# Kernel optimization log

Measured on AMD Instinct MI355X. Metric: run time of the kernel, lower is better.

## Reference

```python
import jax, jax.numpy as jnp
import numpy as np

N_ORDER = 256
PRED_LEN = 192
SEQ_LEN = 768
ENC_IN = 21
BATCH = 16
MULTISCALE = [1, 2, 4]
MODES = 32  # min(32, min(pred_len, seq_len)//2)


def _transition(N):
    Q = np.arange(N, dtype=np.float64)
    R = (2 * Q + 1)[:, None]
    j, i = np.meshgrid(Q, Q)
    A = np.where(i < j, -1, (-1.0) ** (i - j + 1)) * R
    B = (-1.0) ** Q[:, None] * R
    return A, B


def _bilinear(A, B, dt):
    # scipy cont2discrete(method='bilinear'): Ad=(I-dt/2 A)^-1 (I+dt/2 A), Bd=(I-dt/2 A)^-1 dt B
    N = A.shape[0]
    I = np.eye(N)
    ima = I - (dt / 2.0) * A
    Ad = np.linalg.solve(ima, I + (dt / 2.0) * A)
    Bd = np.linalg.solve(ima, dt * B)
    return Ad, Bd.squeeze(-1)


def _legendre_eval(N, x):
    # Legendre P_n(x) via three-term recurrence; returns [len(x), N]
    T = x.shape[0]
    P = np.zeros((N, T))
    P[0] = 1.0
    if N > 1:
        P[1] = x
    for n in range(2, N):
        P[n] = ((2 * n - 1) * x * P[n - 1] - (n - 1) * P[n - 2]) / n
    return P.T


def setup_inputs() -> dict:
    key = jax.random.key(0)
    ks = jax.random.split(key, 12)
    inp = {"x_enc": jax.random.normal(ks[0], (BATCH, SEQ_LEN, ENC_IN), dtype=jnp.float32)}
    Ac, Bc = _transition(N_ORDER)
    scale = 1.0 / (N_ORDER * N_ORDER)
    for idx, m in enumerate(MULTISCALE):
        dt = 1.0 / PRED_LEN / m
        Ad, Bd = _bilinear(Ac, Bc, dt)
        vals = np.arange(0.0, 1.0, dt)
        E = _legendre_eval(N_ORDER, 1.0 - 2.0 * vals)
        inp[f"A{idx}"] = jnp.asarray(Ad, jnp.float32)
        inp[f"B{idx}"] = jnp.asarray(Bd, jnp.float32)
        inp[f"E{idx}"] = jnp.asarray(E, jnp.float32)
        inp[f"Wr{idx}"] = scale * jax.random.uniform(ks[1 + 2 * idx], (N_ORDER, N_ORDER, MODES), dtype=jnp.float32)
        inp[f"Wi{idx}"] = scale * jax.random.uniform(ks[2 + 2 * idx], (N_ORDER, N_ORDER, MODES), dtype=jnp.float32)
    inp["mlp_w"] = 0.1 * jax.random.normal(ks[10], (1, len(MULTISCALE)), dtype=jnp.float32)
    inp["mlp_b"] = jnp.zeros((1,), jnp.float32)
    return inp


def _hippo(x, A, Bv):
    # x: [B, E, L]; c_t = c_{t-1} @ A^T + f_t * B  (F.linear(c, A) == c @ A.T)
    def step(c, f):
        c = c @ A.T + f[..., None] * Bv
        return c, c
    c0 = jnp.zeros(x.shape[:-1] + (A.shape[0],), x.dtype)
    _, cs = jax.lax.scan(step, c0, jnp.moveaxis(x, -1, 0))
    return jnp.moveaxis(cs, 0, -1)  # [B, E, N, L]


def _spec_conv(x, Wr, Wi):
    # x: [B, E, N_in, L]; keep first MODES rfft modes, complex channel mix, irfft
    L = x.shape[-1]
    a = jnp.fft.rfft(x, axis=-1)[..., :MODES]
    W = (Wr + 1j * Wi).astype(jnp.complex64)
    out = jnp.einsum('bjix,iox->bjox', a, W)
    nf = L // 2 + 1
    out_full = jnp.pad(out, ((0, 0), (0, 0), (0, 0), (0, nf - MODES)))
    return jnp.fft.irfft(out_full, n=L, axis=-1)


def reference(x_enc, A0, B0, E0, Wr0, Wi0, A1, B1, E1, Wr1, Wi1, A2, B2, E2, Wr2, Wi2, mlp_w, mlp_b):
    params = [(A0, B0, E0, Wr0, Wi0), (A1, B1, E1, Wr1, Wi1), (A2, B2, E2, Wr2, Wi2)]
    x_decs = []
    for m, (A, Bv, E, Wr, Wi) in zip(MULTISCALE, params):
        x_in = x_enc[:, -m * PRED_LEN:]                      # [B, L, E]
        c = _hippo(jnp.transpose(x_in, (0, 2, 1)), A, Bv)    # [B, E, N, L]
        out1 = _spec_conv(c, Wr, Wi)                         # [B, E, N, L]
        x_dec_c = out1[:, :, :, PRED_LEN - 1]                # seq_len >= pred_len, jump_dist=0
        x_decs.append(x_dec_c @ E[-PRED_LEN:].T)             # [B, E, pred_len]
    x_dec = jnp.stack(x_decs, axis=-1)                       # [B, E, pred_len, 3]
    out = x_dec @ mlp_w[0] + mlp_b[0]                        # Linear(3,1) then squeeze
    return jnp.transpose(out, (0, 2, 1))                     # [B, pred_len, E]
```

## Files before the change

### kernel.cpp

```cpp
#include <hip/hip_runtime.h>
#include <math.h>

#define PI_F 3.14159265358979323846f

#define W_OFF    0
#define AP_OFF   344064
#define KT_OFF   737280
#define KTOT_OFF 995328
#define Y_OFF    1142784
#define S_OFF    1142784
#define F_OFF    1732608
#define QT_OFF   10579968
#define WS_FLOATS 27095040

__device__ __forceinline__ int off_w_f(int s)  { return 49152  * ((1 << s) - 1); }
__device__ __forceinline__ int qoff_f(int s)   { return 2359296 * ((1 << s) - 1); }
__device__ __forceinline__ int foff_f(int s)   { return 1179648 * ((1 << s) - 1); }

template<bool BT>
__device__ __forceinline__ void gemm_tile32(const float* __restrict__ A,
                                            const float* __restrict__ B,
                                            float* __restrict__ C,
                                            int M, int ldc, int m0, int n0)
{
    __shared__ float As[16][36];
    __shared__ float Bs[16][68];
    const int tid = threadIdx.x;
    const int tx = tid & 15;
    const int ty = tid >> 4;

    float acc[2][4] = {{0.f,0.f,0.f,0.f},{0.f,0.f,0.f,0.f}};

    for (int kk = 0; kk < 256; kk += 16) {
        if (tid < 128) {
            int r  = tid >> 2;
            int kq = (tid & 3) << 2;
            float4 av = make_float4(0.f, 0.f, 0.f, 0.f);
            if (m0 + r < M)
                av = *(const float4*)(A + (size_t)(m0 + r) * 256 + kk + kq);
            As[kq + 0][r] = av.x; As[kq + 1][r] = av.y;
            As[kq + 2][r] = av.z; As[kq + 3][r] = av.w;
        }
        if (BT) {
            int rb = tid >> 2;
            int kq = (tid & 3) << 2;
            float4 bv = *(const float4*)(B + (size_t)(n0 + rb) * 256 + kk + kq);
            Bs[kq + 0][rb] = bv.x; Bs[kq + 1][rb] = bv.y;
            Bs[kq + 2][rb] = bv.z; Bs[kq + 3][rb] = bv.w;
        } else {
            int kb = tid >> 4;
            int j4 = (tid & 15) << 2;
            float4 bv = *(const float4*)(B + (size_t)(kk + kb) * 256 + n0 + j4);
            *(float4*)(&Bs[kb][j4]) = bv;
        }
        __syncthreads();

        #pragma unroll
        for (int kq = 0; kq < 16; ++kq) {
            float a0 = As[kq][2 * ty];
            float a1 = As[kq][2 * ty + 1];
            float4 b4 = *(const float4*)(&Bs[kq][tx << 2]);
            acc[0][0] = fmaf(a0, b4.x, acc[0][0]);
            acc[0][1] = fmaf(a0, b4.y, acc[0][1]);
            acc[0][2] = fmaf(a0, b4.z, acc[0][2]);
            acc[0][3] = fmaf(a0, b4.w, acc[0][3]);
            acc[1][0] = fmaf(a1, b4.x, acc[1][0]);
            acc[1][1] = fmaf(a1, b4.y, acc[1][1]);
            acc[1][2] = fmaf(a1, b4.z, acc[1][2]);
            acc[1][3] = fmaf(a1, b4.w, acc[1][3]);
        }
        __syncthreads();
    }

    #pragma unroll
    for (int u = 0; u < 2; ++u) {
        int row = m0 + 2 * ty + u;
        if (row < M) {
            float4 cv = make_float4(acc[u][0], acc[u][1], acc[u][2], acc[u][3]);
            *(float4*)(C + (size_t)row * ldc + n0 + (tx << 2)) = cv;
        }
    }
}

__device__ __forceinline__ void gemm64x128_q(const float* __restrict__ A,
                                             const float* __restrict__ B,
                                             float* __restrict__ C, int ldc)
{
    __shared__ float As[16][68];
    __shared__ float Bs[16][132];

    const int tid = threadIdx.x;
    const int tx = tid & 15;
    const int ty = tid >> 4;
    const int ra  = tid >> 2;
    const int kqa = (tid & 3) << 2;
    const int rb  = tid >> 1;
    const int kq8 = (tid & 1) << 3;

    float acc[2][4][4];
    #pragma unroll
    for (int g = 0; g < 2; ++g)
        #pragma unroll
        for (int u = 0; u < 4; ++u)
            #pragma unroll
            for (int v = 0; v < 4; ++v) acc[g][u][v] = 0.f;

    for (int kk = 0; kk < 256; kk += 16) {
        float4 av = *(const float4*)(A + (size_t)ra * 256 + kk + kqa);
        As[kqa + 0][ra] = av.x; As[kqa + 1][ra] = av.y;
        As[kqa + 2][ra] = av.z; As[kqa + 3][ra] = av.w;

        const float* bp = B + (size_t)rb * 256 + kk + kq8;
        float4 b0 = *(const float4*)(bp);
        float4 b1 = *(const float4*)(bp + 4);
        Bs[kq8 + 0][rb] = b0.x; Bs[kq8 + 1][rb] = b0.y;
        Bs[kq8 + 2][rb] = b0.z; Bs[kq8 + 3][rb] = b0.w;
        Bs[kq8 + 4][rb] = b1.x; Bs[kq8 + 5][rb] = b1.y;
        Bs[kq8 + 6][rb] = b1.z; Bs[kq8 + 7][rb] = b1.w;
        __syncthreads();

        #pragma unroll
        for (int kq = 0; kq < 16; ++kq) {
            float4 a   = *(const float4*)(&As[kq][4 * ty]);
            float4 b0v = *(const float4*)(&Bs[kq][4 * tx]);
            float4 b1v = *(const float4*)(&Bs[kq][4 * tx + 64]);
            float af[4] = {a.x, a.y, a.z, a.w};
            float bf[8] = {b0v.x, b0v.y, b0v.z, b0v.w, b1v.x, b1v.y, b1v.z, b1v.w};
            #pragma unroll
            for (int g = 0; g < 2; ++g)
                #pragma unroll
                for (int u = 0; u < 4; ++u)
                    #pragma unroll
                    for (int v = 0; v < 4; ++v)
                        acc[g][u][v] = fmaf(af[u], bf[g * 4 + v], acc[g][u][v]);
        }
        __syncthreads();
    }

    #pragma unroll
    for (int u = 0; u < 4; ++u) {
        int row = 4 * ty + u;
        #pragma unroll
        for (int g = 0; g < 2; ++g) {
            float4 cv = make_float4(acc[g][u][0], acc[g][u][1],
                                    acc[g][u][2], acc[g][u][3]);
            *(float4*)(C + (size_t)row * ldc + 4 * tx + 64 * g) = cv;
        }
    }
}

__global__ void k_level2(int n, int sbase, const float* A0, const float* A1,
                         const float* A2, const float* B0, const float* B1,
                         const float* B2, float* ws)
{
    int s = blockIdx.z + sbase;
    int L = 192 << s;
    const float* Ain = (s == 0) ? A0 : (s == 1) ? A1 : A2;
    const float* Bv  = (s == 0) ? B0 : (s == 1) ? B1 : B2;
    float* wbase = ws + W_OFF + off_w_f(s);
    float* bufA  = ws + AP_OFF + s * 131072;
    float* bufB  = bufA + 65536;
    const float* src = (n == 0) ? Ain : (((n - 1) & 1) ? bufB : bufA);

    const int y = blockIdx.y;
    const int n0col = blockIdx.x * 64;

    if (n == 0 && y == 15 && blockIdx.x == 3)
        ws[W_OFF + off_w_f(s) + threadIdx.x] = Bv[threadIdx.x];

    if (y < 8) {
        int p2 = 1 << n;
        if (p2 >= L) return;
        int cnt = min(p2, L - p2);
        int m0 = y * 32;
        if (m0 >= cnt) return;
        const float* Aop = (n == 0) ? Bv : wbase;
        gemm_tile32<true>(Aop, src, wbase + (size_t)p2 * 256, cnt, 256, m0, n0col);
    } else {
        if ((2 << n) >= L) return;
        float* dst = (n & 1) ? bufB : bufA;
        gemm_tile32<false>(src, src, dst, 256, 256, (y - 8) * 32, n0col);
    }
}

__global__ void k_transpose(const float* Wr0, const float* Wi0,
                            const float* Wr1, const float* Wi1,
                            const float* Wr2, const float* Wi2, float* ws)
{
    __shared__ float t[256][33];
    int bid = blockIdx.x;
    int i  = bid & 255;
    int ri = (bid >> 8) & 1;
    int s  = bid >> 9;
    const float* W;
    if (s == 0)      W = ri ? Wi0 : Wr0;
    else if (s == 1) W = ri ? Wi1 : Wr1;
    else             W = ri ? Wi2 : Wr2;

    const int tid = threadIdx.x;
    const float* slab = W + (size_t)i * 8192;
    #pragma unroll
    for (int j = 0; j < 8; ++j) {
        int f = j * 1024 + tid * 4;
        float4 v = *(const float4*)(slab + f);
        int o = f >> 5;
        int k = f & 31;
        t[o][k + 0] = v.x; t[o][k + 1] = v.y;
        t[o][k + 2] = v.z; t[o][k + 3] = v.w;
    }
    __syncthreads();

    int sri = s * 2 + ri;
    #pragma unroll
    for (int k = 0; k < 32; ++k) {
        ws[QT_OFF + (size_t)(sri * 32 + k) * 65536 + (size_t)i * 256 + tid] = t[tid][k];
    }
}

__global__ void __launch_bounds__(256, 4)
k_gemm_Y5(const float* E0, const float* E1, const float* E2, float* __restrict__ ws)
{
    const int z  = blockIdx.z;
    const int s  = z >> 6;
    const int L  = 192 << s;
    const int n0 = blockIdx.x * 128;
    const int m0 = blockIdx.y * 64;
    const float* E = (s == 0) ? E0 : (s == 1) ? E1 : E2;

    const float* Ap = E + (size_t)(L - 192) * 256 + (size_t)m0 * 256;
    const float* Bp = ws + QT_OFF + (size_t)z * 65536 + (size_t)n0 * 256;
    float* Cp = ws + Y_OFF + (size_t)z * 49152 + (size_t)m0 * 256 + n0;
    gemm64x128_q(Ap, Bp, Cp, 256);
}

__global__ void __launch_bounds__(256, 4)
k_gemm_Q4(float* __restrict__ ws)
{
    const int y = blockIdx.y;
    int s, yt;
    if (y < 3)      { s = 0; yt = y; }
    else if (y < 9) { s = 1; yt = y - 3; }
    else            { s = 2; yt = y - 9; }
    const int m0 = yt * 64;
    const int n0 = blockIdx.x * 128;

    const float* Ap = ws + W_OFF + off_w_f(s) + (size_t)m0 * 256;
    const float* Bp = ws + Y_OFF + (size_t)s * 3145728 + (size_t)n0 * 256;
    float* Cp = ws + QT_OFF + qoff_f(s) + (size_t)m0 * 12288 + n0;
    gemm64x128_q(Ap, Bp, Cp, 12288);
}

__global__ void k_scanA(float* __restrict__ ws)
{
    const int c = blockIdx.x;
    const int k = blockIdx.y;
    const int s = blockIdx.z;
    const int L = 192 << s;
    const int C = L >> 4;
    const int p = threadIdx.x;

    __shared__ float twc[768], tws[768];
    for (int m = p; m < L; m += 192) {
        float ang = -2.f * PI_F * (float)m / (float)L;
        float ss, cc; sincosf(ang, &ss, &cc);
        twc[m] = cc; tws[m] = ss;
    }
    __syncthreads();

    const float* Qr = ws + QT_OFF + qoff_f(s) + (size_t)k * 192;
    const float* Qi = Qr + 6144;

    float ar = 0.f, ai = 0.f;
    const int d0 = c * C;
    int ph = (k * d0) % L;
    for (int j = 0; j < C; ++j) {
        int d = d0 + j;
        float qr = Qr[(size_t)d * 12288 + p];
        float qi = Qi[(size_t)d * 12288 + p];
        float cc = twc[ph], sn = tws[ph];
        ar = fmaf(cc, qr, fmaf(-sn, qi, ar));
        ai = fmaf(cc, qi, fmaf( sn, qr, ai));
        ph += k; if (ph >= L) ph -= L;
    }
    size_t sb = (size_t)((s * 32 + k) * 16 + c) * 384;
    ws[S_OFF + sb + p]       = ar;
    ws[S_OFF + sb + 192 + p] = ai;
}

__global__ void k_scanB(float* __restrict__ ws)
{
    const int c = blockIdx.x;
    const int k = blockIdx.y;
    const int s = blockIdx.z;
    const int L = 192 << s;
    const int C = L >> 4;
    const int p = threadIdx.x;

    __shared__ float twc[768], tws[768];
    for (int m = p; m < L; m += 192) {
        float ang = -2.f * PI_F * (float)m / (float)L;
        float ss, cc; sincosf(ang, &ss, &cc);
        twc[m] = cc; tws[m] = ss;
    }
    __syncthreads();

    float ar = 0.f, ai = 0.f;
    size_t sbase = (size_t)(s * 32 + k) * 16 * 384;
    for (int c2 = 0; c2 < c; ++c2) {
        ar += ws[S_OFF + sbase + (size_t)c2 * 384 + p];
        ai += ws[S_OFF + sbase + (size_t)c2 * 384 + 192 + p];
    }

    const float ck = ((k == 0) ? 1.f : 2.f) / (float)L;
    const float* Qr = ws + QT_OFF + qoff_f(s) + (size_t)k * 192;
    const float* Qi = Qr + 6144;
    float* F = ws + F_OFF + foff_f(s);

    const int d0 = c * C;
    int ph = (k * d0) % L;
    int m1 = d0 + 192 - L; if (m1 < 0) m1 += L;
    int ph2 = (k * m1) % L;
    for (int j = 0; j < C; ++j) {
        int d = d0 + j;
        float qr = Qr[(size_t)d * 12288 + p];
        float qi = Qi[(size_t)d * 12288 + p];
        float cc = twc[ph], sn = tws[ph];
        ar = fmaf(cc, qr, fmaf(-sn, qi, ar));
        ai = fmaf(cc, qi, fmaf( sn, qr, ai));
        float f = ck * fmaf(twc[ph2], ar, tws[ph2] * ai);
        int sidx = L - 1 - d;
        F[((size_t)sidx * 32 + k) * 192 + p] = f;
        ph  += k; if (ph  >= L) ph  -= L;
        ph2 += k; if (ph2 >= L) ph2 -= L;
    }
}

__global__ void k_kredc(float* __restrict__ ws, const float* __restrict__ mw)
{
    const int tau = blockIdx.x;
    const int p   = threadIdx.x;
    float sum = 0.f;
    #pragma unroll
    for (int s = 0; s < 3; ++s) {
        int L = 192 << s;
        int off = 768 - L;
        if (tau >= off) {
            int sidx = tau - off;
            const float* F = ws + F_OFF + foff_f(s) + (size_t)sidx * 32 * 192;
            float kt = 0.f;
            #pragma unroll
            for (int k = 0; k < 32; ++k)
                kt += F[k * 192 + p];
            sum = fmaf(mw[s], kt, sum);
        }
    }
    ws[KTOT_OFF + (size_t)tau * 192 + p] = sum;
}

__global__ void k_out(const float* __restrict__ x, const float* __restrict__ ws,
                      const float* __restrict__ mb, float* __restrict__ out)
{
    int bid = blockIdx.x;
    int b = bid / 21;
    int c = bid - b * 21;
    __shared__ float xl[768];
    for (int t = threadIdx.x; t < 768; t += 192)
        xl[t] = x[((size_t)b * 768 + t) * 21 + c];
    __syncthreads();

    int p = threadIdx.x;
    const float* K = ws + KTOT_OFF;
    float acc = 0.f;
    for (int tau = 0; tau < 768; ++tau)
        acc = fmaf(xl[tau], K[(size_t)tau * 192 + p], acc);
    out[((size_t)b * 192 + p) * 21 + c] = acc + mb[0];
}

extern "C" void kernel_launch(void* const* d_in, const int* in_sizes, int n_in,
                              void* d_out, int out_size, void* d_ws, size_t ws_size,
                              hipStream_t stream)
{
    const float* x   = (const float*)d_in[0];
    const float* A0  = (const float*)d_in[1];
    const float* B0  = (const float*)d_in[2];
    const float* E0  = (const float*)d_in[3];
    const float* Wr0 = (const float*)d_in[4];
    const float* Wi0 = (const float*)d_in[5];
    const float* A1  = (const float*)d_in[6];
    const float* B1  = (const float*)d_in[7];
    const float* E1  = (const float*)d_in[8];
    const float* Wr1 = (const float*)d_in[9];
    const float* Wi1 = (const float*)d_in[10];
    const float* A2  = (const float*)d_in[11];
    const float* B2  = (const float*)d_in[12];
    const float* E2  = (const float*)d_in[13];
    const float* Wr2 = (const float*)d_in[14];
    const float* Wi2 = (const float*)d_in[15];
    const float* mw  = (const float*)d_in[16];
    const float* mb  = (const float*)d_in[17];
    float* ws  = (float*)d_ws;
    float* out = (float*)d_out;

    if (ws_size < (size_t)WS_FLOATS * sizeof(float)) {
        hipMemsetAsync(d_out, 0, (size_t)out_size * sizeof(float), stream);
        return;
    }

    for (int n = 0; n < 8; ++n)
        k_level2<<<dim3(4, 16, 3), 256, 0, stream>>>(n, 0, A0, A1, A2, B0, B1, B2, ws);
    k_level2<<<dim3(4, 16, 2), 256, 0, stream>>>(8, 1, A0, A1, A2, B0, B1, B2, ws);
    k_level2<<<dim3(4, 16, 1), 256, 0, stream>>>(9, 2, A0, A1, A2, B0, B1, B2, ws);
    k_transpose<<<1536, 256, 0, stream>>>(Wr0, Wi0, Wr1, Wi1, Wr2, Wi2, ws);
    k_gemm_Y5<<<dim3(2, 3, 192), 256, 0, stream>>>(E0, E1, E2, ws);
    k_gemm_Q4<<<dim3(96, 21), 256, 0, stream>>>(ws);
    k_scanA<<<dim3(16, 32, 3), 192, 0, stream>>>(ws);
    k_scanB<<<dim3(16, 32, 3), 192, 0, stream>>>(ws);
    k_kredc<<<768, 192, 0, stream>>>(ws, mw);
    k_out<<<336, 192, 0, stream>>>(x, ws, mb, out);
}
```

Measured before the change: 400.4 us.

## Overlap weight transpose and E-projection GEMMs with the doubling-level launches

Merges the level-doubling kernel, the W transpose and the E×Q GEMM into one kernel. Extra z-slices of each level launch run independent work: the transpose during level 0 and 24 slices of the Y GEMM during each later level. This fills the idle CUs left by the small level GEMMs and removes two separate launches. In exchange the fused kernel has a larger shared-memory footprint and loses the 4-blocks-per-CU launch bound the Y GEMM had, and many blocks exit early.

```diff
diff --git a/kernel.cpp b/kernel.cpp
--- a/kernel.cpp
+++ b/kernel.cpp
@@ -149,46 +149,11 @@
     }
 }
 
-__global__ void k_level2(int n, int sbase, const float* A0, const float* A1,
-                         const float* A2, const float* B0, const float* B1,
-                         const float* B2, float* ws)
-{
-    int s = blockIdx.z + sbase;
-    int L = 192 << s;
-    const float* Ain = (s == 0) ? A0 : (s == 1) ? A1 : A2;
-    const float* Bv  = (s == 0) ? B0 : (s == 1) ? B1 : B2;
-    float* wbase = ws + W_OFF + off_w_f(s);
-    float* bufA  = ws + AP_OFF + s * 131072;
-    float* bufB  = bufA + 65536;
-    const float* src = (n == 0) ? Ain : (((n - 1) & 1) ? bufB : bufA);
-
-    const int y = blockIdx.y;
-    const int n0col = blockIdx.x * 64;
-
-    if (n == 0 && y == 15 && blockIdx.x == 3)
-        ws[W_OFF + off_w_f(s) + threadIdx.x] = Bv[threadIdx.x];
-
-    if (y < 8) {
-        int p2 = 1 << n;
-        if (p2 >= L) return;
-        int cnt = min(p2, L - p2);
-        int m0 = y * 32;
-        if (m0 >= cnt) return;
-        const float* Aop = (n == 0) ? Bv : wbase;
-        gemm_tile32<true>(Aop, src, wbase + (size_t)p2 * 256, cnt, 256, m0, n0col);
-    } else {
-        if ((2 << n) >= L) return;
-        float* dst = (n & 1) ? bufB : bufA;
-        gemm_tile32<false>(src, src, dst, 256, 256, (y - 8) * 32, n0col);
-    }
-}
-
-__global__ void k_transpose(const float* Wr0, const float* Wi0,
-                            const float* Wr1, const float* Wi1,
-                            const float* Wr2, const float* Wi2, float* ws)
+__device__ __forceinline__ void transpose_body(int bid,
+    const float* Wr0, const float* Wi0, const float* Wr1, const float* Wi1,
+    const float* Wr2, const float* Wi2, float* ws)
 {
     __shared__ float t[256][33];
-    int bid = blockIdx.x;
     int i  = bid & 255;
     int ri = (bid >> 8) & 1;
     int s  = bid >> 9;
@@ -217,20 +182,68 @@
     }
 }
 
-__global__ void __launch_bounds__(256, 4)
-k_gemm_Y5(const float* E0, const float* E1, const float* E2, float* __restrict__ ws)
-{
-    const int z  = blockIdx.z;
-    const int s  = z >> 6;
-    const int L  = 192 << s;
-    const int n0 = blockIdx.x * 128;
-    const int m0 = blockIdx.y * 64;
+__device__ __forceinline__ void y_body(int yz, int n0, int m0,
+    const float* E0, const float* E1, const float* E2, float* ws)
+{
+    const int s = yz >> 6;
+    const int L = 192 << s;
     const float* E = (s == 0) ? E0 : (s == 1) ? E1 : E2;
-
     const float* Ap = E + (size_t)(L - 192) * 256 + (size_t)m0 * 256;
-    const float* Bp = ws + QT_OFF + (size_t)z * 65536 + (size_t)n0 * 256;
-    float* Cp = ws + Y_OFF + (size_t)z * 49152 + (size_t)m0 * 256 + n0;
+    const float* Bp = ws + QT_OFF + (size_t)yz * 65536 + (size_t)n0 * 256;
+    float* Cp = ws + Y_OFF + (size_t)yz * 49152 + (size_t)m0 * 256 + n0;
     gemm64x128_q(Ap, Bp, Cp, 256);
+}
+
+__global__ void __launch_bounds__(256)
+k_level3(int n, int sbase, int nz_lev, int ylo,
+         const float* A0, const float* A1, const float* A2,
+         const float* B0, const float* B1, const float* B2,
+         const float* E0, const float* E1, const float* E2,
+         const float* Wr0, const float* Wi0, const float* Wr1, const float* Wi1,
+         const float* Wr2, const float* Wi2, float* ws)
+{
+    const int z = blockIdx.z;
+    if (z < nz_lev) {
+        int s = z + sbase;
+        int L = 192 << s;
+        const float* Ain = (s == 0) ? A0 : (s == 1) ? A1 : A2;
+        const float* Bv  = (s == 0) ? B0 : (s == 1) ? B1 : B2;
+        float* wbase = ws + W_OFF + off_w_f(s);
+        float* bufA  = ws + AP_OFF + s * 131072;
+        float* bufB  = bufA + 65536;
+        const float* src = (n == 0) ? Ain : (((n - 1) & 1) ? bufB : bufA);
+
+        const int y = blockIdx.y;
+        const int n0col = blockIdx.x * 64;
+
+        if (n == 0 && y == 15 && blockIdx.x == 3)
+            ws[W_OFF + off_w_f(s) + threadIdx.x] = Bv[threadIdx.x];
+
+        if (y < 8) {
+            int p2 = 1 << n;
+            if (p2 >= L) return;
+            int cnt = min(p2, L - p2);
+            int m0 = y * 32;
+            if (m0 >= cnt) return;
+            const float* Aop = (n == 0) ? Bv : wbase;
+            gemm_tile32<true>(Aop, src, wbase + (size_t)p2 * 256, cnt, 256, m0, n0col);
+        } else {
+            if ((2 << n) >= L) return;
+            float* dst = (n & 1) ? bufB : bufA;
+            gemm_tile32<false>(src, src, dst, 256, 256, (y - 8) * 32, n0col);
+        }
+        return;
+    }
+
+    if (n == 0) {
+        int bid = (z - nz_lev) * 64 + blockIdx.y * 4 + blockIdx.x;
+        transpose_body(bid, Wr0, Wi0, Wr1, Wi1, Wr2, Wi2, ws);
+        return;
+    }
+
+    if (blockIdx.x >= 2 || blockIdx.y >= 3) return;
+    int yz = ylo + (z - nz_lev);
+    y_body(yz, blockIdx.x * 128, blockIdx.y * 64, E0, E1, E2, ws);
 }
 
 __global__ void __launch_bounds__(256, 4)
@@ -406,12 +419,16 @@
         return;
     }
 
-    for (int n = 0; n < 8; ++n)
-        k_level2<<<dim3(4, 16, 3), 256, 0, stream>>>(n, 0, A0, A1, A2, B0, B1, B2, ws);
-    k_level2<<<dim3(4, 16, 2), 256, 0, stream>>>(8, 1, A0, A1, A2, B0, B1, B2, ws);
-    k_level2<<<dim3(4, 16, 1), 256, 0, stream>>>(9, 2, A0, A1, A2, B0, B1, B2, ws);
-    k_transpose<<<1536, 256, 0, stream>>>(Wr0, Wi0, Wr1, Wi1, Wr2, Wi2, ws);
-    k_gemm_Y5<<<dim3(2, 3, 192), 256, 0, stream>>>(E0, E1, E2, ws);
+    k_level3<<<dim3(4, 16, 27), 256, 0, stream>>>(0, 0, 3, 0,
+        A0, A1, A2, B0, B1, B2, E0, E1, E2, Wr0, Wi0, Wr1, Wi1, Wr2, Wi2, ws);
+    for (int n = 1; n < 8; ++n)
+        k_level3<<<dim3(4, 16, 27), 256, 0, stream>>>(n, 0, 3, 24 * (n - 1),
+            A0, A1, A2, B0, B1, B2, E0, E1, E2, Wr0, Wi0, Wr1, Wi1, Wr2, Wi2, ws);
+    k_level3<<<dim3(4, 16, 26), 256, 0, stream>>>(8, 1, 2, 168,
+        A0, A1, A2, B0, B1, B2, E0, E1, E2, Wr0, Wi0, Wr1, Wi1, Wr2, Wi2, ws);
+    k_level3<<<dim3(4, 16, 1), 256, 0, stream>>>(9, 2, 1, 0,
+        A0, A1, A2, B0, B1, B2, E0, E1, E2, Wr0, Wi0, Wr1, Wi1, Wr2, Wi2, ws);
+
     k_gemm_Q4<<<dim3(96, 21), 256, 0, stream>>>(ws);
     k_scanA<<<dim3(16, 32, 3), 192, 0, stream>>>(ws);
     k_scanB<<<dim3(16, 32, 3), 192, 0, stream>>>(ws);
```

Result: slower. 594.0 us (+48.4%).
